# Optimization experiments

Hardware: AMD Instinct MI355X
Metric: run time of the kernel (lower is better)

Reference implementation:

```python
import jax, jax.numpy as jnp
import numpy as np
from jax import lax

D_MODEL = 512
INPUT_DIM = 64
D_INNER = 1024      # expand * d_model
D_STATE = 128
NHEADS = 16         # d_inner // headdim (headdim = ssm_state//num_heads = 64)
HEADDIM = 64
D_CONV = 4
CONV_DIM = D_INNER + 2 * D_STATE          # 1280 (ngroups=1)
D_IN_PROJ = 2 * D_INNER + 2 * D_STATE + NHEADS  # 2320
BATCH = 2
SEQ = 1024
MASK_RATIO = 0.75
EPS = 1e-5


def setup_inputs() -> dict:
    key = jax.random.key(0)
    ks = jax.random.split(key, 14)
    s = lambda fan: 1.0 / np.sqrt(fan)
    return {
        "x": jax.random.normal(ks[0], (BATCH, SEQ, INPUT_DIM), jnp.float32),
        "conv_emb_w": jax.random.normal(ks[1], (D_MODEL, INPUT_DIM, 3), jnp.float32) * s(INPUT_DIM * 3),
        "conv_emb_b": jax.random.normal(ks[2], (D_MODEL,), jnp.float32) * 0.02,
        "cls_token": jax.random.normal(ks[3], (1, 1, D_MODEL), jnp.float32) * 0.02,
        "in_proj_w": jax.random.normal(ks[4], (D_IN_PROJ, D_MODEL), jnp.float32) * s(D_MODEL),
        "conv1d_w": jax.random.normal(ks[5], (CONV_DIM, 1, D_CONV), jnp.float32) * s(D_CONV),
        "conv1d_b": jax.random.normal(ks[6], (CONV_DIM,), jnp.float32) * 0.02,
        "dt_bias": jax.random.uniform(ks[7], (NHEADS,), jnp.float32, -4.0, 0.0),
        "A_log": jnp.log(jax.random.uniform(ks[8], (NHEADS,), jnp.float32, 1.0, 16.0)),
        "D": jax.random.normal(ks[9], (NHEADS,), jnp.float32),
        "rms_w": jnp.ones((D_INNER,), jnp.float32),
        "out_proj_w": jax.random.normal(ks[10], (D_MODEL, D_INNER), jnp.float32) * s(D_INNER),
        "ln_g": jnp.ones((D_MODEL,), jnp.float32),
        "ln_b": jnp.zeros((D_MODEL,), jnp.float32),
    }


def _forward(x, conv_emb_w, conv_emb_b, cls_token, in_proj_w, conv1d_w, conv1d_b,
             dt_bias, A_log, D, rms_w, out_proj_w, ln_g, ln_b):
    b = x.shape[0]
    # ---- conv embedding: Conv1d(k=3, pad=1) over time ----
    xe = lax.conv_general_dilated(x.transpose(0, 2, 1), conv_emb_w, (1,), [(1, 1)],
                                  dimension_numbers=("NCH", "OIH", "NCH"))
    xe = (xe + conv_emb_b[None, :, None]).transpose(0, 2, 1)  # (b, L, d_model)
    # ---- append CLS token at end ----
    h = jnp.concatenate([xe, jnp.broadcast_to(cls_token, (b, 1, D_MODEL))], axis=1)
    L = h.shape[1]
    # ---- Mamba2 block ----
    zxbcdt = jnp.einsum("bld,ed->ble", h, in_proj_w)  # (b, L, 2320)
    z = zxbcdt[..., :D_INNER]
    xBC = zxbcdt[..., D_INNER:D_INNER + CONV_DIM]
    dt = jax.nn.softplus(zxbcdt[..., -NHEADS:] + dt_bias)  # (b, L, h)
    # causal depthwise conv (pad left d_conv-1) + SiLU
    xBC = lax.conv_general_dilated(xBC.transpose(0, 2, 1), conv1d_w, (1,), [(D_CONV - 1, 0)],
                                   dimension_numbers=("NCH", "OIH", "NCH"),
                                   feature_group_count=CONV_DIM)
    xBC = jax.nn.silu((xBC + conv1d_b[None, :, None]).transpose(0, 2, 1))  # (b, L, 1280)
    x_in = xBC[..., :D_INNER].reshape(b, L, NHEADS, HEADDIM)   # (b, L, h, p)
    B = xBC[..., D_INNER:D_INNER + D_STATE]                     # (b, L, n)
    C = xBC[..., D_INNER + D_STATE:]                            # (b, L, n)
    A = -jnp.exp(A_log)                                         # (h,)
    dA = jnp.exp(dt * A)                                        # (b, L, h)
    # selective state-space scan; state (b, h, p, n)
    def step(state, inp):
        x_t, dt_t, B_t, C_t, dA_t = inp  # (b,h,p) (b,h) (b,n) (b,n) (b,h)
        state = state * dA_t[:, :, None, None] + \
            (dt_t[:, :, None] * x_t)[..., None] * B_t[:, None, None, :]
        y_t = jnp.einsum("bhpn,bn->bhp", state, C_t)
        return state, y_t
    s0 = jnp.zeros((b, NHEADS, HEADDIM, D_STATE), x.dtype)
    _, ys = lax.scan(step, s0, (x_in.transpose(1, 0, 2, 3), dt.transpose(1, 0, 2),
                                B.transpose(1, 0, 2), C.transpose(1, 0, 2),
                                dA.transpose(1, 0, 2)))
    y = ys.transpose(1, 0, 2, 3) + D[None, None, :, None] * x_in  # (b, L, h, p)
    y = y.reshape(b, L, D_INNER)
    # gated RMSNorm: gate first, then normalize
    y = y * jax.nn.silu(z)
    y = y * lax.rsqrt(jnp.mean(y * y, axis=-1, keepdims=True) + EPS) * rms_w
    out = jnp.einsum("ble,de->bld", y, out_proj_w)  # (b, L, d_model)
    # ---- LayerNorm ----
    mu = jnp.mean(out, axis=-1, keepdims=True)
    var = jnp.mean((out - mu) ** 2, axis=-1, keepdims=True)
    out = (out - mu) * lax.rsqrt(var + EPS) * ln_g + ln_b
    return out


def reference(x, conv_emb_w, conv_emb_b, cls_token, in_proj_w, conv1d_w, conv1d_b,
              dt_bias, A_log, D, rms_w, out_proj_w, ln_g, ln_b):
    out = _forward(x, conv_emb_w, conv_emb_b, cls_token, in_proj_w, conv1d_w, conv1d_b,
                   dt_bias, A_log, D, rms_w, out_proj_w, ln_g, ln_b)
    b = out.shape[0]
    cls = out[:, -1:, :]
    body = out[:, :-1, :]                      # (b, SEQ, d)
    len_keep = int(SEQ * (1 - MASK_RATIO))     # 256
    noise = jax.random.uniform(jax.random.fold_in(jax.random.key(0), 1), (b, SEQ))
    ids_shuffle = jnp.argsort(noise, axis=1)
    ids_restore = jnp.argsort(ids_shuffle, axis=1)
    ids_keep = ids_shuffle[:, :len_keep]
    x_masked = jnp.take_along_axis(body, ids_keep[:, :, None], axis=1)
    mask = jnp.where(jnp.arange(SEQ)[None, :] < len_keep, 0.0, 1.0)
    mask = jnp.take_along_axis(jnp.broadcast_to(mask, (b, SEQ)), ids_restore, axis=1)
    x_out = jnp.concatenate([x_masked, cls], axis=1)  # (b, len_keep+1, d)
    return (x_out, mask, ids_restore, ids_keep)
```

## Files before the change

kernel.cpp:

```cpp
#include <hip/hip_runtime.h>
#include <hip/hip_bf16.h>
#include <stdint.h>

#define LTOK  1025
#define NROWS 2050
#define DM    512
#define DIN   1024
#define DST   128
#define NHEAD 16
#define HDIM  64
#define CDIM  1280
#define EPROJ 2320
#define QC    64
#define NCH   17

#define O_RIDX   0
#define O_CB     1024
#define O_CLS    1536
#define O_C1B    2048
#define O_DTB    3328
#define O_ALOG   3344
#define O_DV     3360
#define O_RMSW   3376
#define O_LNG    4400
#define O_LNB    4912
#define O_CW     5440
#define O_IPW    103744
#define O_OPW    1291584
#define O_C1W    1815872
#define O_CX     1820992
#define O_ZX     1952064
#define O_XBC    6708064
#define O_DT     9332064
#define O_LGA    9364864
#define O_Y      9397664
#define O_X3     10447264
#define O_OUTG   11496864
#define O_SL     11760032
#define O_CLA    16216480
#define O_SL2    16251296
#define O_KEEP   18479520
#define O_OUTP   18480128
#define O_CWT    19532800
#define O_W2     19581952
#define O_BIAS2  19804672

#define OO_MASK 263168
#define OO_IDR  265216
#define OO_IDK  267264

typedef __attribute__((ext_vector_type(8))) short short8;
typedef __attribute__((ext_vector_type(8))) unsigned short ushortx8;
typedef __attribute__((ext_vector_type(4))) float floatx4;

__device__ __forceinline__ short f2bs(float f) {
  union { float f; uint32_t u; } v; v.f = f;
  uint32_t r = (v.u + 0x7FFFu + ((v.u >> 16) & 1u)) >> 16;
  return (short)r;
}
__device__ __forceinline__ float bf2f(uint16_t u) {
  return __uint_as_float(((uint32_t)u) << 16);
}

struct InPtrs { const void* p[14]; };

__device__ __forceinline__ uint32_t rotl32(uint32_t v, int d) {
  return (v << d) | (v >> (32 - d));
}
__device__ void threefry2x32(uint32_t k0, uint32_t k1, uint32_t c0, uint32_t c1,
                             uint32_t& o0, uint32_t& o1) {
  uint32_t ks0 = k0, ks1 = k1, ks2 = 0x1BD11BDAu ^ k0 ^ k1;
  uint32_t x0 = c0 + ks0, x1 = c1 + ks1;
#define TF_R4(a,b,c,d) \
  x0 += x1; x1 = rotl32(x1,a); x1 ^= x0; \
  x0 += x1; x1 = rotl32(x1,b); x1 ^= x0; \
  x0 += x1; x1 = rotl32(x1,c); x1 ^= x0; \
  x0 += x1; x1 = rotl32(x1,d); x1 ^= x0;
  TF_R4(13,15,26,6)  x0 += ks1; x1 += ks2 + 1u;
  TF_R4(17,29,16,24) x0 += ks2; x1 += ks0 + 2u;
  TF_R4(13,15,26,6)  x0 += ks0; x1 += ks1 + 3u;
  TF_R4(17,29,16,24) x0 += ks1; x1 += ks2 + 4u;
  TF_R4(13,15,26,6)  x0 += ks2; x1 += ks0 + 5u;
#undef TF_R4
  o0 = x0; o1 = x1;
}

__device__ int detect_is_f32(const uint32_t* w, int nelem) {
  int nw = nelem / 2; if (nw > 16) nw = 16;
  int insane = 0, lozero = 0, anynz = 0;
  for (int i = 0; i < nw; ++i) {
    uint32_t word = w[i];
    if (word != 0u) anynz = 1;
    uint32_t lo = word & 0xffffu;
    if (lo == 0u) { lozero++; continue; }
    float v = __uint_as_float(lo << 16);
    float a = fabsf(v);
    if (!(a >= 1e-8f && a <= 1e4f)) insane++;
  }
  if (insane >= 2) return 1;
  if (lozero == nw && anynz) return 1;
  return 0;
}

__global__ __launch_bounds__(256) void k_convert(InPtrs ptrs, float* ws,
                                                 float* out, int* rowidx) {
  static const int sizes[13] = {98304, 512, 512, 1187840, 5120, 1280,
                                16, 16, 16, 1024, 524288, 512, 512};
  static const int offs[13]  = {O_CW, O_CB, O_CLS, O_IPW, O_C1W, O_C1B,
                                O_DTB, O_ALOG, O_DV, O_RMSW, O_OPW, O_LNG, O_LNB};
  static const int isbf[13]  = {1,0,0,1,0,0,0,0,0,0,1,0,0};
  static const int smallT[15] = {1,2,4,4,4,4,4,5,5,6,7,8,9,11,12};
  static const int smallB[15] = {0,0,0,1,2,3,4,0,1,0,0,0,0,0,0};
  int bx = blockIdx.x;
  int tid = threadIdx.x;

  if (bx < 256) {
    const uint32_t* xp = (const uint32_t*)ptrs.p[0];
    __shared__ int xf;
    if (tid == 0) xf = detect_is_f32(xp, 131072);
    __syncthreads();
    if (tid < 192) {
      int r = bx * 8 + tid / 24;
      int seg = tid % 24;
      int kk = seg >> 3, i0 = (seg & 7) * 8;
      int b = r >> 10, idx = r & 1023;
      int tt = idx + kk - 1;
      ushortx8 o = {0,0,0,0,0,0,0,0};
      if (tt >= 0 && tt < 1024) {
        long src = ((long)(b * 1024 + tt)) * 64 + i0;
        if (xf) {
          const float* xfp = (const float*)xp;
          float4 f0 = *(const float4*)(xfp + src);
          float4 f1 = *(const float4*)(xfp + src + 4);
          o[0] = (uint16_t)f2bs(f0.x); o[1] = (uint16_t)f2bs(f0.y);
          o[2] = (uint16_t)f2bs(f0.z); o[3] = (uint16_t)f2bs(f0.w);
          o[4] = (uint16_t)f2bs(f1.x); o[5] = (uint16_t)f2bs(f1.y);
          o[6] = (uint16_t)f2bs(f1.z); o[7] = (uint16_t)f2bs(f1.w);
        } else {
          o = *(const ushortx8*)((const uint16_t*)xp + src);
        }
      }
      *(ushortx8*)((uint16_t*)(ws + O_X3) + (long)r * 192 + kk * 64 + i0) = o;
    }
    return;
  }
  bx -= 256;

  int t, blk;
  if (bx < 1160) { t = 3; blk = bx; }
  else {
    bx -= 1160;
    if (bx < 512) { t = 10; blk = bx; }
    else {
      bx -= 512;
      if (bx < 96) {
        const uint32_t* w = (const uint32_t*)ptrs.p[1];
        __shared__ int sf;
        if (tid == 0) sf = detect_is_f32(w, 98304);
        __syncthreads();
        int base = (bx * 256 + tid) * 4;
        if (base >= 98304) return;
        uint16_t vv[4];
        if (sf) {
          const float4 f = *(const float4*)((const float*)w + base);
          vv[0] = (uint16_t)f2bs(f.x); vv[1] = (uint16_t)f2bs(f.y);
          vv[2] = (uint16_t)f2bs(f.z); vv[3] = (uint16_t)f2bs(f.w);
        } else {
          const uint32_t* s = w + (base >> 1);
          uint32_t w0 = s[0], w1 = s[1];
          vv[0] = (uint16_t)(w0 & 0xffffu); vv[1] = (uint16_t)(w0 >> 16);
          vv[2] = (uint16_t)(w1 & 0xffffu); vv[3] = (uint16_t)(w1 >> 16);
        }
        int o = base / 192, ik = base % 192;
        uint16_t* cwt = (uint16_t*)(ws + O_CWT);
#pragma unroll
        for (int j = 0; j < 4; ++j) {
          int ikj = ik + j;
          int kp = (ikj % 3) * 64 + (ikj / 3);
          cwt[(long)kp * 512 + o] = vv[j];
        }
        return;
      }
      bx -= 96;
      if (bx < 32) {
        int seg = bx & 15, b = bx >> 4;
        uint8_t* keep = (uint8_t*)(ws + O_KEEP);
        __shared__ float vals[1024];
        uint32_t fk0, fk1;
        threefry2x32(0u, 0u, 0u, 1u, fk0, fk1);
#pragma unroll
        for (int k = 0; k < 4; ++k) {
          int i = tid + k * 256;
          uint32_t o0, o1;
          threefry2x32(fk0, fk1, 0u, (uint32_t)(b * 1024 + i), o0, o1);
          uint32_t bits = o0 ^ o1;
          vals[i] = __uint_as_float((bits >> 9) | 0x3f800000u) - 1.0f;
        }
        __syncthreads();
        int tg = seg * 64 + (tid >> 2);
        int qq = tid & 3;
        float v = vals[tg];
        int r = 0;
        int j0 = qq * 256;
        for (int it = 0; it < 256; ++it) {
          int j = j0 + ((it + qq * 8) & 255);
          float vj = vals[j];
          r += (vj < v || (vj == v && j < tg)) ? 1 : 0;
        }
        r += __shfl_xor(r, 1, 64);
        r += __shfl_xor(r, 2, 64);
        if (qq == 0) {
          out[OO_IDR + b * 1024 + tg] = (float)r;
          out[OO_MASK + b * 1024 + tg] = (r < 256) ? 0.0f : 1.0f;
          keep[b * LTOK + tg] = (r < 256) ? 1 : 0;
          if (r < 256) {
            out[OO_IDK + b * 256 + r] = (float)tg;
            rowidx[b * 257 + r] = b * LTOK + tg;
          }
          if (tg == 0) {
            rowidx[b * 257 + 256] = b * LTOK + 1024;
            keep[b * LTOK + 1024] = 1;
          }
        }
        return;
      }
      bx -= 32;
      if (bx >= 15) return;
      t = smallT[bx]; blk = smallB[bx];
    }
  }

  int n = sizes[t];
  const uint32_t* w = (const uint32_t*)ptrs.p[t + 1];
  __shared__ int sf;
  if (tid == 0) sf = detect_is_f32(w, n);
  __syncthreads();
  int base = (blk * 256 + tid) * 4;
  if (base >= n) return;
  if (isbf[t]) {
    ushort4 o;
    if (sf) {
      const float4 vv = *(const float4*)((const float*)w + base);
      o.x = (uint16_t)f2bs(vv.x); o.y = (uint16_t)f2bs(vv.y);
      o.z = (uint16_t)f2bs(vv.z); o.w = (uint16_t)f2bs(vv.w);
    } else {
      const uint32_t* s = w + (base >> 1);
      uint32_t w0 = s[0], w1 = s[1];
      o.x = (uint16_t)(w0 & 0xffffu); o.y = (uint16_t)(w0 >> 16);
      o.z = (uint16_t)(w1 & 0xffffu); o.w = (uint16_t)(w1 >> 16);
    }
    *(ushort4*)((uint16_t*)(ws + offs[t]) + base) = o;
  } else {
    float* dst = ws + offs[t];
    if (sf) {
      *(float4*)(dst + base) = *(const float4*)((const float*)w + base);
    } else {
      const uint32_t* s = w + (base >> 1);
      uint32_t w0 = s[0], w1 = s[1];
      float4 o;
      o.x = __uint_as_float((w0 & 0xffffu) << 16);
      o.y = __uint_as_float(w0 & 0xffff0000u);
      o.z = __uint_as_float((w1 & 0xffffu) << 16);
      o.w = __uint_as_float(w1 & 0xffff0000u);
      *(float4*)(dst + base) = o;
    }
  }
}

__global__ __launch_bounds__(256) void k_w2(const uint16_t* __restrict__ IPW,
                                            const uint16_t* __restrict__ CWT,
                                            const float* __restrict__ cb,
                                            const float* __restrict__ cls,
                                            uint16_t* __restrict__ W2,
                                            float* __restrict__ bias2,
                                            uint16_t* __restrict__ ZX) {
  int bx = blockIdx.x;
  int tid = threadIdx.x;

  if (bx >= 111) {
    __shared__ float scb[512];
    __shared__ float scl[512];
    for (int i = tid; i < 512; i += 256) {
      scb[i] = cb[i];
      scl[i] = bf2f((uint16_t)f2bs(cls[i]));
    }
    __syncthreads();
    int e = (bx - 111) * 232 + tid;
    if (tid < 232 && e < 2320) {
      float sb = 0.f, sc = 0.f;
      for (int d8 = 0; d8 < 512; d8 += 8) {
        ushortx8 v = *(const ushortx8*)(IPW + (long)e * 512 + d8);
#pragma unroll
        for (int j = 0; j < 8; ++j) {
          float wv = bf2f(v[j]);
          sb = fmaf(wv, scb[d8 + j], sb);
          sc = fmaf(wv, scl[d8 + j], sc);
        }
      }
      bias2[e] = sb;
      uint16_t cz = (uint16_t)f2bs(sc);
      ZX[(long)1024 * EPROJ + e] = cz;
      ZX[(long)2049 * EPROJ + e] = cz;
    }
    return;
  }

  int bm = bx / 3, bn = bx % 3;
  __shared__ __align__(16) short sA[64 * 264];
  __shared__ __align__(16) short sB[64 * 264];
  int lane = tid & 63, w = tid >> 6, lm = lane & 15, q = lane >> 4;

  floatx4 acc[4] = {};
  for (int ph = 0; ph < 2; ++ph) {
    int d0 = ph * 256;
#pragma unroll
    for (int it = 0; it < 8; ++it) {
      int li = it * 256 + tid;
      int row = li >> 5, col = (li & 31) * 8;
      int ge = bm * 64 + row;
      ushortx8 av = {0,0,0,0,0,0,0,0};
      if (ge < 2320) av = *(const ushortx8*)(IPW + (long)ge * 512 + d0 + col);
      *(ushortx8*)&sA[row * 264 + col] = av;
      ushortx8 bv = *(const ushortx8*)(CWT + (long)(bn * 64 + row) * 512 + d0 + col);
      *(ushortx8*)&sB[row * 264 + col] = bv;
    }
    __syncthreads();
#pragma unroll
    for (int kk = 0; kk < 8; ++kk) {
      short8 a = *(const short8*)&sA[(w * 16 + lm) * 264 + kk * 32 + q * 8];
#pragma unroll
      for (int ct = 0; ct < 4; ++ct) {
        short8 b = *(const short8*)&sB[(ct * 16 + lm) * 264 + kk * 32 + q * 8];
        acc[ct] = __builtin_amdgcn_mfma_f32_16x16x32_bf16(a, b, acc[ct], 0, 0, 0);
      }
    }
    __syncthreads();
  }
#pragma unroll
  for (int reg = 0; reg < 4; ++reg) {
    int e = bm * 64 + w * 16 + q * 4 + reg;
    if (e < 2320) {
#pragma unroll
      for (int ct = 0; ct < 4; ++ct)
        W2[(long)e * 192 + bn * 64 + ct * 16 + lm] = (uint16_t)f2bs(acc[ct][reg]);
    }
  }
}

__global__ __launch_bounds__(256) void k_ipgemm(const uint16_t* __restrict__ X3,
                                                const uint16_t* __restrict__ W2,
                                                const float* __restrict__ bias2,
                                                const uint8_t* __restrict__ keep,
                                                uint16_t* __restrict__ ZX) {
  __shared__ __align__(16) short sA[64 * 200];
  __shared__ __align__(16) short sB[64 * 200];
  __shared__ uint8_t skp[64];
  int tid = threadIdx.x;
  int lane = tid & 63, w = tid >> 6, lm = lane & 15, q = lane >> 4;
  int bm = blockIdx.y * 64, bn = blockIdx.x * 64;

  if (tid < 64) {
    int rr = bm + tid;
    skp[tid] = keep[(rr >> 10) * LTOK + (rr & 1023)];
  }
#pragma unroll
  for (int it = 0; it < 6; ++it) {
    int li = it * 256 + tid;
    int row = li / 24, col = (li % 24) * 8;
    ushortx8 av = *(const ushortx8*)(X3 + (long)(bm + row) * 192 + col);
    *(ushortx8*)&sA[row * 200 + col] = av;
    int gn = bn + row;
    ushortx8 bv = {0,0,0,0,0,0,0,0};
    if (gn < 2320) bv = *(const ushortx8*)(W2 + (long)gn * 192 + col);
    *(ushortx8*)&sB[row * 200 + col] = bv;
  }
  __syncthreads();

  floatx4 acc[4] = {};
#pragma unroll
  for (int kb = 0; kb < 6; ++kb) {
    short8 a = *(const short8*)&sA[(w * 16 + lm) * 200 + kb * 32 + q * 8];
#pragma unroll
    for (int ct = 0; ct < 4; ++ct) {
      short8 b = *(const short8*)&sB[(ct * 16 + lm) * 200 + kb * 32 + q * 8];
      acc[ct] = __builtin_amdgcn_mfma_f32_16x16x32_bf16(a, b, acc[ct], 0, 0, 0);
    }
  }
#pragma unroll
  for (int reg = 0; reg < 4; ++reg) {
    int r = bm + w * 16 + q * 4 + reg;
    long crow = (long)((r >> 10) * LTOK + (r & 1023));
    int kp = skp[r - bm];
#pragma unroll
    for (int ct = 0; ct < 4; ++ct) {
      int e = bn + ct * 16 + lm;
      if (e < 2320 && (e >= DIN || kp))
        ZX[crow * EPROJ + e] = (uint16_t)f2bs(acc[ct][reg] + bias2[e]);
    }
  }
}

__global__ __launch_bounds__(320) void k_conv1d(const uint16_t* __restrict__ zx,
                                                const float* __restrict__ w,
                                                const float* __restrict__ bias,
                                                uint16_t* __restrict__ xbc,
                                                const float* __restrict__ dtb,
                                                const float* __restrict__ alog,
                                                float* __restrict__ dt,
                                                float* __restrict__ lga) {
  int g = blockIdx.x;
  int tid = threadIdx.x;
  if (g >= 514) {
    if (tid < 256) {
      int idx = (g - 514) * 256 + tid;
      if (idx < NROWS * NHEAD) {
        int rr = idx >> 4, h = idx & 15;
        float xv = bf2f(zx[(long)rr * EPROJ + (EPROJ - NHEAD) + h]) + dtb[h];
        float dtv = (xv > 20.f) ? xv : log1pf(expf(xv));
        dt[idx] = dtv;
        lga[idx] = dtv * (-expf(alog[h]));
      }
    }
    return;
  }
  {
    int xcd = g & 7, slot = g >> 3;
    g = (xcd < 2) ? xcd * 65 + slot : 130 + (xcd - 2) * 64 + slot;
  }
  int b = g / 257, gi = g % 257;
  int t0 = gi * 4;
  int nr = (t0 == 1024) ? 1 : 4;
  const uint16_t* zrow = zx + (long)b * LTOK * EPROJ + DIN;
  int c4 = tid * 4;
  {
    float4 bi = *(const float4*)(bias + c4);
    float4 w0 = *(const float4*)(w + (c4 + 0) * 4);
    float4 w1 = *(const float4*)(w + (c4 + 1) * 4);
    float4 w2 = *(const float4*)(w + (c4 + 2) * 4);
    float4 w3 = *(const float4*)(w + (c4 + 3) * 4);
    float wr[4][4] = {{w0.x, w0.y, w0.z, w0.w}, {w1.x, w1.y, w1.z, w1.w},
                      {w2.x, w2.y, w2.z, w2.w}, {w3.x, w3.y, w3.z, w3.w}};
    float acc[4][4];
#pragma unroll
    for (int ri = 0; ri < 4; ++ri) {
      acc[ri][0] = bi.x; acc[ri][1] = bi.y; acc[ri][2] = bi.z; acc[ri][3] = bi.w;
    }
#pragma unroll
    for (int dtt = -3; dtt <= 3; ++dtt) {
      int tt = t0 + dtt;
      if (tt < 0 || tt > 1024) continue;
      ushort4 xv = *(const ushort4*)(zrow + (long)tt * EPROJ + c4);
      float x0 = bf2f(xv.x), x1 = bf2f(xv.y), x2 = bf2f(xv.z), x3 = bf2f(xv.w);
#pragma unroll
      for (int ri = 0; ri < 4; ++ri) {
        int k = dtt - ri + 3;
        if (k >= 0 && k <= 3) {
          acc[ri][0] = fmaf(wr[0][k], x0, acc[ri][0]);
          acc[ri][1] = fmaf(wr[1][k], x1, acc[ri][1]);
          acc[ri][2] = fmaf(wr[2][k], x2, acc[ri][2]);
          acc[ri][3] = fmaf(wr[3][k], x3, acc[ri][3]);
        }
      }
    }
#pragma unroll
    for (int ri = 0; ri < 4; ++ri) {
      if (ri < nr) {
        long r = (long)b * LTOK + t0 + ri;
        ushort4 o;
        o.x = (uint16_t)f2bs(acc[ri][0] / (1.f + __expf(-acc[ri][0])));
        o.y = (uint16_t)f2bs(acc[ri][1] / (1.f + __expf(-acc[ri][1])));
        o.z = (uint16_t)f2bs(acc[ri][2] / (1.f + __expf(-acc[ri][2])));
        o.w = (uint16_t)f2bs(acc[ri][3] / (1.f + __expf(-acc[ri][3])));
        *(ushort4*)(xbc + r * CDIM + c4) = o;
      }
    }
  }
}

__global__ __launch_bounds__(256) void k_ssd1(const uint16_t* __restrict__ xbc,
                                              const float* __restrict__ dt,
                                              const float* __restrict__ lga,
                                              uint16_t* __restrict__ SL,
                                              float* __restrict__ CLA) {
  int blk = blockIdx.x;
  int c = blk % NCH;
  int hh = blk / NCH;
  int h = hh & 15, b = hh >> 4;
  int tid = threadIdx.x;
  int lane = tid & 63, w = tid >> 6;
  int lm = lane & 15, q = lane >> 4;

  __shared__ __align__(16) short sBT[128 * 72];
  __shared__ __align__(16) short sXT[64 * 72];
  __shared__ float wwv[64];

  int t0 = c * QC;
  const uint16_t* base = xbc + (long)b * LTOK * CDIM;

  if (tid < 64) {
    int t = t0 + tid;
    float dtv = (t < LTOK) ? dt[((long)(b * LTOK + t)) * NHEAD + h] : 0.f;
    float v   = (t < LTOK) ? lga[((long)(b * LTOK + t)) * NHEAD + h] : 0.f;
#pragma unroll
    for (int off = 1; off < 64; off <<= 1) {
      float u = __shfl_up(v, off, 64);
      if (lane >= off) v += u;
    }
    float clEnd = __shfl(v, 63, 64);
    wwv[tid] = __expf(clEnd - v) * dtv;
    CLA[(long)blk * 64 + tid] = v;
  }
  ushort4 bvr[8];
#pragma unroll
  for (int k = 0; k < 8; ++k) {
    int e4 = (tid + k * 256) * 4;
    int row = e4 >> 7, col = e4 & 127;
    int t = t0 + row;
    ushort4 bv = {0,0,0,0};
    if (t < LTOK) bv = *(const ushort4*)(base + (long)t * CDIM + DIN + col);
    bvr[k] = bv;
  }
#pragma unroll
  for (int k = 0; k < 4; ++k) {
    int e4 = (tid + k * 256) * 4;
    int row = e4 >> 6, col = e4 & 63;
    int t = t0 + row;
    ushort4 xv = {0,0,0,0};
    if (t < LTOK) xv = *(const ushort4*)(base + (long)t * CDIM + h * 64 + col);
    sXT[(col  )*72+row]=(short)xv.x; sXT[(col+1)*72+row]=(short)xv.y;
    sXT[(col+2)*72+row]=(short)xv.z; sXT[(col+3)*72+row]=(short)xv.w;
  }
  __syncthreads();

#pragma unroll
  for (int k = 0; k < 8; ++k) {
    int e4 = (tid + k * 256) * 4;
    int row = e4 >> 7, col = e4 & 127;
    ushort4 bv = bvr[k];
    float wv = wwv[row];
    sBT[(col  )*72+row]=f2bs(bf2f(bv.x)*wv); sBT[(col+1)*72+row]=f2bs(bf2f(bv.y)*wv);
    sBT[(col+2)*72+row]=f2bs(bf2f(bv.z)*wv); sBT[(col+3)*72+row]=f2bs(bf2f(bv.w)*wv);
  }
  __syncthreads();

  floatx4 s[2][4] = {};
#pragma unroll
  for (int kb = 0; kb < 2; ++kb) {
    short8 bfr[4];
#pragma unroll
    for (int ct = 0; ct < 4; ++ct)
      bfr[ct] = *(const short8*)&sXT[(ct*16 + lm)*72 + kb*32 + q*8];
#pragma unroll
    for (int nt = 0; nt < 2; ++nt) {
      short8 a = *(const short8*)&sBT[((w*2+nt)*16 + lm)*72 + kb*32 + q*8];
#pragma unroll
      for (int ct = 0; ct < 4; ++ct)
        s[nt][ct] = __builtin_amdgcn_mfma_f32_16x16x32_bf16(a, bfr[ct], s[nt][ct], 0, 0, 0);
    }
  }
  uint16_t* slp = SL + (long)blk * 8192;
#pragma unroll
  for (int nt = 0; nt < 2; ++nt)
#pragma unroll
    for (int ct = 0; ct < 4; ++ct)
#pragma unroll
      for (int reg = 0; reg < 4; ++reg) {
        int n = (w*2+nt)*16 + q*4 + reg;
        int p = ct*16 + lm;
        slp[n*64 + p] = (uint16_t)f2bs(s[nt][ct][reg]);
      }
}

__global__ __launch_bounds__(256) void k_comb(const uint16_t* __restrict__ SL,
                                              const float* __restrict__ CLA,
                                              uint16_t* __restrict__ SL2) {
  int bx = blockIdx.x;
  int piece = bx & 15;
  int hh = bx >> 4;
  int off = piece * 512 + threadIdx.x * 2;
  long cb0 = (long)hh * NCH;
  float P[NCH];
  float2 tmp[NCH];
#pragma unroll
  for (int c = 0; c < NCH; ++c) {
    P[c] = __expf(CLA[(cb0 + c) * 64 + 63]);
    uint32_t pk = *(const uint32_t*)(SL + (cb0 + c) * 8192 + off);
    tmp[c].x = bf2f((uint16_t)(pk & 0xffffu));
    tmp[c].y = bf2f((uint16_t)(pk >> 16));
  }
  float2 s = make_float2(0.f, 0.f);
#pragma unroll
  for (int c = 0; c < NCH; ++c) {
    uint32_t packed = (uint32_t)(uint16_t)f2bs(s.x) | ((uint32_t)(uint16_t)f2bs(s.y) << 16);
    *(uint32_t*)(SL2 + (cb0 + c) * 8192 + off) = packed;
    s.x = fmaf(P[c], s.x, tmp[c].x);
    s.y = fmaf(P[c], s.y, tmp[c].y);
  }
}

__global__ __launch_bounds__(256) void k_ssd3(const uint16_t* __restrict__ xbc,
                                              const float* __restrict__ dt,
                                              const uint16_t* __restrict__ SL2,
                                              const float* __restrict__ CLA,
                                              const uint8_t* __restrict__ keepf,
                                              float* __restrict__ Y) {
  int blk = blockIdx.x;
  int c = blk % NCH;
  int hh = blk / NCH;
  int h = hh & 15, b = hh >> 4;
  int tid = threadIdx.x;
  int lane = tid & 63, w = tid >> 6;
  int lm = lane & 15, q = lane >> 4;

  __shared__ __align__(16) short sST[64 * 136];
  __shared__ __align__(16) short sXT[64 * 72];
  __shared__ __align__(16) short sM[64 * 72];
  __shared__ float dtw[64], clA[64], evec[64];
  __shared__ uint8_t kf[64];

  int t0 = c * QC;
  const uint16_t* base = xbc + (long)b * LTOK * CDIM;
  const uint16_t* slp = SL2 + (long)blk * 8192;

  if (tid < 64) {
    int t = t0 + tid;
    dtw[tid] = (t < LTOK) ? dt[((long)(b * LTOK + t)) * NHEAD + h] : 0.f;
    float v = CLA[(long)blk * 64 + tid];
    clA[tid] = v;
    evec[tid] = __expf(v);
    kf[tid] = (t < LTOK) ? keepf[b * LTOK + t] : 0;
  }

  short8 cfr[4], bb0[4];
  {
    int tA = t0 + w*16 + lm;
    bool tAok = tA < LTOK;
    short8 z = {0,0,0,0,0,0,0,0};
#pragma unroll
    for (int kb = 0; kb < 4; ++kb)
      cfr[kb] = tAok ? *(const short8*)(base + (long)tA * CDIM + DIN + DST + kb*32 + q*8) : z;
#pragma unroll
    for (int ct = 0; ct < 4; ++ct) {
      int tB = t0 + ct*16 + lm;
      bb0[ct] = (tB < LTOK) ? *(const short8*)(base + (long)tB * CDIM + DIN + q*8) : z;
    }
  }

#pragma unroll
  for (int k = 0; k < 4; ++k) {
    int e4 = (tid + k * 256) * 4;
    int row = e4 >> 6, col = e4 & 63;
    int t = t0 + row;
    ushort4 xv = {0,0,0,0};
    if (t < LTOK) xv = *(const ushort4*)(base + (long)t * CDIM + h * 64 + col);
    sXT[(col  )*72+row]=(short)xv.x; sXT[(col+1)*72+row]=(short)xv.y;
    sXT[(col+2)*72+row]=(short)xv.z; sXT[(col+3)*72+row]=(short)xv.w;
  }
#pragma unroll
  for (int k = 0; k < 8; ++k) {
    int e4 = (tid + k * 256) * 4;
    int n = e4 >> 6, p = e4 & 63;
    ushort4 sv = *(const ushort4*)(slp + n * 64 + p);
    sST[(p  )*136+n]=(short)sv.x; sST[(p+1)*136+n]=(short)sv.y;
    sST[(p+2)*136+n]=(short)sv.z; sST[(p+3)*136+n]=(short)sv.w;
  }
  __syncthreads();

  floatx4 g[4] = {};
#pragma unroll
  for (int ct = 0; ct < 4; ++ct)
    g[ct] = __builtin_amdgcn_mfma_f32_16x16x32_bf16(cfr[0], bb0[ct], g[ct], 0, 0, 0);
#pragma unroll
  for (int kb = 1; kb < 4; ++kb) {
#pragma unroll
    for (int ct = 0; ct < 4; ++ct) {
      int tB = t0 + ct*16 + lm;
      short8 z = {0,0,0,0,0,0,0,0};
      short8 bb = (tB < LTOK) ? *(const short8*)(base + (long)tB * CDIM + DIN + kb*32 + q*8) : z;
      g[ct] = __builtin_amdgcn_mfma_f32_16x16x32_bf16(cfr[kb], bb, g[ct], 0, 0, 0);
    }
  }
#pragma unroll
  for (int ct = 0; ct < 4; ++ct) {
    int tp = ct*16 + lm;
#pragma unroll
    for (int reg = 0; reg < 4; ++reg) {
      int tl = w*16 + q*4 + reg;
      float m = 0.f;
      if (tp <= tl) m = g[ct][reg] * __expf(clA[tl] - clA[tp]) * dtw[tp];
      sM[tl*72 + tp] = f2bs(m);
    }
  }
  floatx4 y2[4] = {};
#pragma unroll
  for (int kb = 0; kb < 4; ++kb) {
#pragma unroll
    for (int ct = 0; ct < 4; ++ct) {
      short8 bb = *(const short8*)&sST[(ct*16 + lm)*136 + kb*32 + q*8];
      y2[ct] = __builtin_amdgcn_mfma_f32_16x16x32_bf16(cfr[kb], bb, y2[ct], 0, 0, 0);
    }
  }
  __syncthreads();
  floatx4 y1[4] = {};
#pragma unroll
  for (int kb = 0; kb < 2; ++kb) {
    short8 a = *(const short8*)&sM[(w*16 + lm)*72 + kb*32 + q*8];
#pragma unroll
    for (int ct = 0; ct < 4; ++ct) {
      short8 bb = *(const short8*)&sXT[(ct*16 + lm)*72 + kb*32 + q*8];
      y1[ct] = __builtin_amdgcn_mfma_f32_16x16x32_bf16(a, bb, y1[ct], 0, 0, 0);
    }
  }
#pragma unroll
  for (int reg = 0; reg < 4; ++reg) {
    int tl = w*16 + q*4 + reg;
    int t = t0 + tl;
    if (t < LTOK && kf[tl]) {
      float ev = evec[tl];
#pragma unroll
      for (int ct = 0; ct < 4; ++ct) {
        int p = ct*16 + lm;
        Y[((long)(b * LTOK + t)) * DIN + h * 64 + p] = y1[ct][reg] + ev * y2[ct][reg];
      }
    }
  }
}

__global__ __launch_bounds__(256) void k_gaterms(const float* __restrict__ Y,
                                                 const uint16_t* __restrict__ xbc,
                                                 const uint16_t* __restrict__ zx,
                                                 const float* __restrict__ Dv,
                                                 const float* __restrict__ rmsw,
                                                 const int* __restrict__ ridx,
                                                 uint16_t* __restrict__ G) {
  int rr = blockIdx.x;
  long r = ridx[rr];
  int tid = threadIdx.x;
  int e = tid * 4;
  int h = tid >> 4;
  float4 a = *(const float4*)(Y + r * DIN + e);
  const ushort4 xu = *(const ushort4*)(xbc + r * CDIM + e);
  const ushort4 zu = *(const ushort4*)(zx + r * EPROJ + e);
  float Dh = Dv[h];
  float y0 = a.x + Dh * bf2f(xu.x), y1 = a.y + Dh * bf2f(xu.y);
  float y2 = a.z + Dh * bf2f(xu.z), y3 = a.w + Dh * bf2f(xu.w);
  float z0 = bf2f(zu.x), z1 = bf2f(zu.y), z2 = bf2f(zu.z), z3 = bf2f(zu.w);
  float g0 = y0 * (z0 / (1.f + __expf(-z0)));
  float g1 = y1 * (z1 / (1.f + __expf(-z1)));
  float g2 = y2 * (z2 / (1.f + __expf(-z2)));
  float g3 = y3 * (z3 / (1.f + __expf(-z3)));
  __shared__ float red[256];
  red[tid] = g0*g0 + g1*g1 + g2*g2 + g3*g3;
  __syncthreads();
  for (int st = 128; st; st >>= 1) {
    if (tid < st) red[tid] += red[tid + st];
    __syncthreads();
  }
  float scale = rsqrtf(red[0] * (1.0f / 1024.0f) + 1e-5f);
  float4 rw = *(const float4*)(rmsw + e);
  ushort4 o;
  o.x = (uint16_t)f2bs(g0 * scale * rw.x);
  o.y = (uint16_t)f2bs(g1 * scale * rw.y);
  o.z = (uint16_t)f2bs(g2 * scale * rw.z);
  o.w = (uint16_t)f2bs(g3 * scale * rw.w);
  *(ushort4*)(G + (long)rr * DIN + e) = o;
}

__global__ __launch_bounds__(256) void k_ogemm(const uint16_t* __restrict__ A,
                                               const uint16_t* __restrict__ Bw,
                                               float* __restrict__ OUTP) {
  __shared__ __align__(16) short sA[64 * 264];
  __shared__ __align__(16) short sB[64 * 264];
  int tid = threadIdx.x;
  int lane = tid & 63, w = tid >> 6;
  int lm = lane & 15, q = lane >> 4;
  int bm = blockIdx.y * 64, bn = blockIdx.x * 64;
  int kbase = blockIdx.z * 256;

#pragma unroll
  for (int it = 0; it < 8; ++it) {
    int li = it * 256 + tid;
    int row = li >> 5, col = (li & 31) * 8;
    int gm = bm + row;
    ushortx8 av = {0,0,0,0,0,0,0,0};
    if (gm < 514) av = *(const ushortx8*)(A + (long)gm * 1024 + kbase + col);
    *(ushortx8*)&sA[row * 264 + col] = av;
    ushortx8 bv = *(const ushortx8*)(Bw + (long)(bn + row) * 1024 + kbase + col);
    *(ushortx8*)&sB[row * 264 + col] = bv;
  }
  __syncthreads();

  floatx4 acc[4] = {};
#pragma unroll
  for (int kb = 0; kb < 8; ++kb) {
    short8 a = *(const short8*)&sA[(w * 16 + lm) * 264 + kb * 32 + q * 8];
#pragma unroll
    for (int ct = 0; ct < 4; ++ct) {
      short8 b = *(const short8*)&sB[(ct * 16 + lm) * 264 + kb * 32 + q * 8];
      acc[ct] = __builtin_amdgcn_mfma_f32_16x16x32_bf16(a, b, acc[ct], 0, 0, 0);
    }
  }
  float* op = OUTP + (long)blockIdx.z * 263168;
#pragma unroll
  for (int reg = 0; reg < 4; ++reg) {
    int r = bm + w * 16 + q * 4 + reg;
    if (r < 514) {
#pragma unroll
      for (int ct = 0; ct < 4; ++ct)
        op[(long)r * 512 + bn + ct * 16 + lm] = acc[ct][reg];
    }
  }
}

__global__ __launch_bounds__(256) void k_ln(const float* __restrict__ outp,
                                            const float* __restrict__ lng,
                                            const float* __restrict__ lnb,
                                            float* __restrict__ out) {
  int r = blockIdx.x;
  int tid = threadIdx.x;
  long e = (long)r * DM + tid * 2;
  float2 v0 = *(const float2*)(outp + e);
  float2 v1 = *(const float2*)(outp + 263168 + e);
  float2 v2 = *(const float2*)(outp + 2 * 263168 + e);
  float2 v3 = *(const float2*)(outp + 3 * 263168 + e);
  float2 v;
  v.x = ((v0.x + v1.x) + v2.x) + v3.x;
  v.y = ((v0.y + v1.y) + v2.y) + v3.y;
  __shared__ float red[256];
  red[tid] = v.x + v.y;
  __syncthreads();
  for (int st = 128; st; st >>= 1) { if (tid < st) red[tid] += red[tid + st]; __syncthreads(); }
  float mu = red[0] * (1.0f / 512.0f);
  __syncthreads();
  float dx = v.x - mu, dy = v.y - mu;
  red[tid] = dx * dx + dy * dy;
  __syncthreads();
  for (int st = 128; st; st >>= 1) { if (tid < st) red[tid] += red[tid + st]; __syncthreads(); }
  float sc = rsqrtf(red[0] * (1.0f / 512.0f) + 1e-5f);
  int c = tid * 2;
  out[(long)r * DM + c]     = dx * sc * lng[c] + lnb[c];
  out[(long)r * DM + c + 1] = dy * sc * lng[c + 1] + lnb[c + 1];
}

extern "C" void kernel_launch(void* const* d_in, const int* in_sizes, int n_in,
                              void* d_out, int out_size, void* d_ws, size_t ws_size,
                              hipStream_t stream) {
  float* ws = (float*)d_ws;
  float* out = (float*)d_out;
  int* rowidx = (int*)(ws + O_RIDX);
  InPtrs ip;
  for (int i = 0; i < 14; ++i) ip.p[i] = d_in[i];

  hipLaunchKernelGGL(k_convert, dim3(2071), dim3(256), 0, stream, ip, ws, out, rowidx);
  hipLaunchKernelGGL(k_w2, dim3(121), dim3(256), 0, stream,
                     (const uint16_t*)(ws + O_IPW), (const uint16_t*)(ws + O_CWT),
                     ws + O_CB, ws + O_CLS,
                     (uint16_t*)(ws + O_W2), ws + O_BIAS2, (uint16_t*)(ws + O_ZX));
  hipLaunchKernelGGL(k_ipgemm, dim3(37, 32), dim3(256), 0, stream,
                     (const uint16_t*)(ws + O_X3), (const uint16_t*)(ws + O_W2),
                     ws + O_BIAS2, (const uint8_t*)(ws + O_KEEP),
                     (uint16_t*)(ws + O_ZX));
  hipLaunchKernelGGL(k_conv1d, dim3(643), dim3(320), 0, stream,
                     (const uint16_t*)(ws + O_ZX), ws + O_C1W, ws + O_C1B,
                     (uint16_t*)(ws + O_XBC),
                     ws + O_DTB, ws + O_ALOG, ws + O_DT, ws + O_LGA);
  hipLaunchKernelGGL(k_ssd1, dim3(32 * NCH), dim3(256), 0, stream,
                     (const uint16_t*)(ws + O_XBC), ws + O_DT, ws + O_LGA,
                     (uint16_t*)(ws + O_SL), ws + O_CLA);
  hipLaunchKernelGGL(k_comb, dim3(512), dim3(256), 0, stream,
                     (const uint16_t*)(ws + O_SL), ws + O_CLA, (uint16_t*)(ws + O_SL2));
  hipLaunchKernelGGL(k_ssd3, dim3(32 * NCH), dim3(256), 0, stream,
                     (const uint16_t*)(ws + O_XBC), ws + O_DT,
                     (const uint16_t*)(ws + O_SL2), ws + O_CLA,
                     (const uint8_t*)(ws + O_KEEP), ws + O_Y);
  hipLaunchKernelGGL(k_gaterms, dim3(514), dim3(256), 0, stream,
                     ws + O_Y, (const uint16_t*)(ws + O_XBC),
                     (const uint16_t*)(ws + O_ZX), ws + O_DV, ws + O_RMSW,
                     (const int*)rowidx, (uint16_t*)(ws + O_X3));
  hipLaunchKernelGGL(k_ogemm, dim3(8, 9, 4), dim3(256), 0, stream,
                     (const uint16_t*)(ws + O_X3), (const uint16_t*)(ws + O_OPW),
                     ws + O_OUTP);
  hipLaunchKernelGGL(k_ln, dim3(514), dim3(256), 0, stream,
                     ws + O_OUTP, ws + O_LNG, ws + O_LNB, out);
}
```

Baseline: 179.4 us.

## Fuse chunk-state combine into ssd1 via per-head atomic counters

```diff
diff --git a/kernel.cpp b/kernel.cpp
--- a/kernel.cpp
+++ b/kernel.cpp
@@ -35,7 +35,7 @@
 #define O_LGA    9364864
 #define O_Y      9397664
 #define O_X3     10447264
-#define O_OUTG   11496864
+#define O_CNT    11496864
 #define O_SL     11760032
 #define O_CLA    16216480
 #define O_SL2    16251296
@@ -225,7 +225,11 @@
         return;
       }
       bx -= 32;
-      if (bx >= 15) return;
+      if (bx == 15) {
+        if (tid < 32) ((int*)(ws + O_CNT))[tid] = 0;
+        return;
+      }
+      if (bx > 15) return;
       t = smallT[bx]; blk = smallB[bx];
     }
   }
@@ -481,12 +485,46 @@
                                               const float* __restrict__ dt,
                                               const float* __restrict__ lga,
                                               uint16_t* __restrict__ SL,
-                                              float* __restrict__ CLA) {
+                                              float* __restrict__ CLA,
+                                              uint16_t* __restrict__ SL2,
+                                              int* __restrict__ cnt) {
   int blk = blockIdx.x;
+  int tid = threadIdx.x;
+
+  if (blk >= 544) {
+    int bx2 = blk - 544;
+    int piece = bx2 & 15;
+    int hh2 = bx2 >> 4;
+    if (tid == 0) {
+      while (atomicAdd(&cnt[hh2], 0) < NCH) __builtin_amdgcn_s_sleep(16);
+      __threadfence();
+    }
+    __syncthreads();
+    int off = piece * 512 + tid * 2;
+    long cb0 = (long)hh2 * NCH;
+    float P[NCH];
+    float2 tmp[NCH];
+#pragma unroll
+    for (int c = 0; c < NCH; ++c) {
+      P[c] = __expf(CLA[(cb0 + c) * 64 + 63]);
+      uint32_t pk = *(const uint32_t*)(SL + (cb0 + c) * 8192 + off);
+      tmp[c].x = bf2f((uint16_t)(pk & 0xffffu));
+      tmp[c].y = bf2f((uint16_t)(pk >> 16));
+    }
+    float2 s = make_float2(0.f, 0.f);
+#pragma unroll
+    for (int c = 0; c < NCH; ++c) {
+      uint32_t packed = (uint32_t)(uint16_t)f2bs(s.x) | ((uint32_t)(uint16_t)f2bs(s.y) << 16);
+      *(uint32_t*)(SL2 + (cb0 + c) * 8192 + off) = packed;
+      s.x = fmaf(P[c], s.x, tmp[c].x);
+      s.y = fmaf(P[c], s.y, tmp[c].y);
+    }
+    return;
+  }
+
   int c = blk % NCH;
   int hh = blk / NCH;
   int h = hh & 15, b = hh >> 4;
-  int tid = threadIdx.x;
   int lane = tid & 63, w = tid >> 6;
   int lm = lane & 15, q = lane >> 4;
 
@@ -569,32 +607,10 @@
         int p = ct*16 + lm;
         slp[n*64 + p] = (uint16_t)f2bs(s[nt][ct][reg]);
       }
-}
-
-__global__ __launch_bounds__(256) void k_comb(const uint16_t* __restrict__ SL,
-                                              const float* __restrict__ CLA,
-                                              uint16_t* __restrict__ SL2) {
-  int bx = blockIdx.x;
-  int piece = bx & 15;
-  int hh = bx >> 4;
-  int off = piece * 512 + threadIdx.x * 2;
-  long cb0 = (long)hh * NCH;
-  float P[NCH];
-  float2 tmp[NCH];
-#pragma unroll
-  for (int c = 0; c < NCH; ++c) {
-    P[c] = __expf(CLA[(cb0 + c) * 64 + 63]);
-    uint32_t pk = *(const uint32_t*)(SL + (cb0 + c) * 8192 + off);
-    tmp[c].x = bf2f((uint16_t)(pk & 0xffffu));
-    tmp[c].y = bf2f((uint16_t)(pk >> 16));
-  }
-  float2 s = make_float2(0.f, 0.f);
-#pragma unroll
-  for (int c = 0; c < NCH; ++c) {
-    uint32_t packed = (uint32_t)(uint16_t)f2bs(s.x) | ((uint32_t)(uint16_t)f2bs(s.y) << 16);
-    *(uint32_t*)(SL2 + (cb0 + c) * 8192 + off) = packed;
-    s.x = fmaf(P[c], s.x, tmp[c].x);
-    s.y = fmaf(P[c], s.y, tmp[c].y);
+  __syncthreads();
+  if (tid == 0) {
+    __threadfence();
+    atomicAdd(&cnt[hh], 1);
   }
 }
 
@@ -851,7 +867,7 @@
   InPtrs ip;
   for (int i = 0; i < 14; ++i) ip.p[i] = d_in[i];
 
-  hipLaunchKernelGGL(k_convert, dim3(2071), dim3(256), 0, stream, ip, ws, out, rowidx);
+  hipLaunchKernelGGL(k_convert, dim3(2072), dim3(256), 0, stream, ip, ws, out, rowidx);
   hipLaunchKernelGGL(k_w2, dim3(121), dim3(256), 0, stream,
                      (const uint16_t*)(ws + O_IPW), (const uint16_t*)(ws + O_CWT),
                      ws + O_CB, ws + O_CLS,
@@ -864,11 +880,10 @@
                      (const uint16_t*)(ws + O_ZX), ws + O_C1W, ws + O_C1B,
                      (uint16_t*)(ws + O_XBC),
                      ws + O_DTB, ws + O_ALOG, ws + O_DT, ws + O_LGA);
-  hipLaunchKernelGGL(k_ssd1, dim3(32 * NCH), dim3(256), 0, stream,
+  hipLaunchKernelGGL(k_ssd1, dim3(1056), dim3(256), 0, stream,
                      (const uint16_t*)(ws + O_XBC), ws + O_DT, ws + O_LGA,
-                     (uint16_t*)(ws + O_SL), ws + O_CLA);
-  hipLaunchKernelGGL(k_comb, dim3(512), dim3(256), 0, stream,
-                     (const uint16_t*)(ws + O_SL), ws + O_CLA, (uint16_t*)(ws + O_SL2));
+                     (uint16_t*)(ws + O_SL), ws + O_CLA,
+                     (uint16_t*)(ws + O_SL2), (int*)(ws + O_CNT));
   hipLaunchKernelGGL(k_ssd3, dim3(32 * NCH), dim3(256), 0, stream,
                      (const uint16_t*)(ws + O_XBC), ws + O_DT,
                      (const uint16_t*)(ws + O_SL2), ws + O_CLA,
```

Measured after the change: 246.2 us. 1.37x slower.
